# Kernel optimization log

Hardware: AMD Instinct MI355X
Metric: run time of the kernel (lower is better)

The kernel has to match this reference:

```python
import jax, jax.numpy as jnp
import numpy as np

B, N, E = 64, 512, 8192          # graphs, nodes per graph, edges per graph
F_IN, H, C = 128, 128, 10        # in features, hidden, classes
K1, K2 = 256, 128                # dense pool cluster counts: ceil(.5*N), ceil(.5*K1)
EPS = 1e-15


def setup_inputs():
    key = jax.random.key(0)
    keys = jax.random.split(key, 32)
    it = iter(keys)
    def w(shape, fan_in):
        return jax.random.normal(next(it), shape, jnp.float32) / np.sqrt(fan_in)
    x = jax.random.normal(next(it), (B * N, F_IN), jnp.float32)
    src_l = jax.random.randint(next(it), (B, E), 0, N)
    dst_l = jax.random.randint(next(it), (B, E), 0, N)
    off = (jnp.arange(B) * N)[:, None]
    src = (src_l + off).reshape(-1).astype(jnp.int32)
    dst = (dst_l + off).reshape(-1).astype(jnp.int32)
    return dict(
        x=x, src=src, dst=dst,
        conv0_wr=w((F_IN, H), F_IN), conv0_wroot=w((F_IN, H), F_IN), conv0_b=jnp.zeros((H,), jnp.float32),
        sconv2_wr=w((H, H), H), sconv2_wroot=w((H, H), H), sconv2_b=jnp.zeros((H,), jnp.float32),
        sconv3_wr=w((H, H), H), sconv3_wroot=w((H, H), H), sconv3_b=jnp.zeros((H,), jnp.float32),
        sage1_wr=w((H, H), H), sage1_wroot=w((H, H), H), sage1_b=jnp.zeros((H,), jnp.float32),
        sage2_wr=w((H, H), H), sage2_wroot=w((H, H), H), sage2_b=jnp.zeros((H,), jnp.float32),
        pool0_w=w((H, K1), H), pool0_b=jnp.zeros((K1,), jnp.float32),
        pool1_w=w((H, K2), H), pool1_b=jnp.zeros((K2,), jnp.float32),
        p1=w((H,), H), p2=w((H,), H), p3=w((H,), H),
        lin1_1_w=w((2 * H, H), 2 * H), lin1_1_b=jnp.zeros((H,), jnp.float32),
        lin1_w=w((H, H), H), lin1_b=jnp.zeros((H,), jnp.float32),
        lin2_w=w((2 * H, C), 2 * H), lin2_b=jnp.zeros((C,), jnp.float32),
    )


def _graph_conv(x, src, dst, emask, wr, wroot, b, n):
    # PyG GraphConv: lin_rel(sum_j x_j) + lin_root(x_i); invalid edges masked to 0.
    msg = x[src] * emask[:, None]
    agg = jax.ops.segment_sum(msg, dst, num_segments=n)
    return agg @ wr + x @ wroot + b


def _topk_pool(x, score_w, src, dst, emask, n_per_graph, k):
    # TopK pooling (MPoolS): score = x.w/||w||, keep top ratio*n per graph, gate by tanh(score).
    score = x @ score_w / (jnp.linalg.norm(score_w) + 1e-16)
    idx = jax.lax.top_k(score.reshape(B, n_per_graph), k)[1]
    perm = (idx + (jnp.arange(B) * n_per_graph)[:, None]).reshape(-1)
    new_x = x[perm] * jnp.tanh(score[perm])[:, None]
    new_id = jnp.full((B * n_per_graph,), -1, jnp.int32).at[perm].set(
        jnp.arange(B * k, dtype=jnp.int32))
    ns, nd = new_id[src], new_id[dst]
    valid = (ns >= 0) & (nd >= 0) & (emask > 0)
    return new_x, jnp.where(valid, ns, 0), jnp.where(valid, nd, 0), valid.astype(x.dtype)


def _readout(x, k):
    # gmp || gap per graph (nodes are contiguous, k per graph)
    xr = x.reshape(B, k, -1)
    return jnp.concatenate([xr.max(axis=1), xr.mean(axis=1)], axis=-1)


def _dense_sage(x, adj, wr, wroot, b):
    agg = (adj @ x) / jnp.clip(adj.sum(-1, keepdims=True), 1.0, None)
    return agg @ wr + x @ wroot + b


def _dense_mincut_pool(x, adj, s):
    s = jax.nn.softmax(s, axis=-1)
    k = s.shape[-1]
    out = jnp.einsum('bnk,bnf->bkf', s, x)
    out_adj = jnp.einsum('bnk,bnm,bml->bkl', s, adj, s)
    mincut_num = jnp.trace(out_adj, axis1=-2, axis2=-1)
    deg = adj.sum(-1)
    mincut_den = jnp.einsum('bn,bnk,bnk->b', deg, s, s)
    mc = -jnp.mean(mincut_num / (mincut_den + EPS))
    ss = jnp.einsum('bnk,bnl->bkl', s, s)
    ss_n = jnp.linalg.norm(ss, axis=(1, 2), keepdims=True)
    eye = jnp.eye(k, dtype=x.dtype)
    o = jnp.mean(jnp.linalg.norm(ss / (ss_n + EPS) - eye / jnp.sqrt(k), axis=(1, 2)))
    di = jnp.arange(k)
    out_adj = out_adj.at[:, di, di].set(0.0)
    dpool = jnp.sqrt(out_adj.sum(-1)) + EPS
    out_adj = out_adj / dpool[:, :, None] / dpool[:, None, :]
    return out, out_adj, mc, o


def _forward(x, src, dst, conv0_wr, conv0_wroot, conv0_b, sconv2_wr, sconv2_wroot, sconv2_b,
             sconv3_wr, sconv3_wroot, sconv3_b, sage1_wr, sage1_wroot, sage1_b,
             sage2_wr, sage2_wroot, sage2_b, pool0_w, pool0_b, pool1_w, pool1_b,
             p1, p2, p3, lin1_1_w, lin1_1_b, lin1_w, lin1_b, lin2_w, lin2_b):
    relu = jax.nn.relu
    e0 = jnp.ones((src.shape[0],), x.dtype)
    x0 = relu(_graph_conv(x, src, dst, e0, conv0_wr, conv0_wroot, conv0_b, B * N))
    # ---- sparse (MPoolS / top-k) branch, stage 1 ----
    sx, s1, d1, m1 = _topk_pool(x0, p1, src, dst, e0, N, N // 2)
    sx1 = _readout(sx, N // 2)
    # ---- dense (DiffPool-style) branch ----
    xd = x0.reshape(B, N, H)                               # to_dense_batch (full mask)
    g = src // N
    adj = jnp.zeros((B, N, N), x.dtype).at[g, src % N, dst % N].add(1.0)  # to_dense_adj
    s = xd @ pool0_w + pool0_b
    xd, adj, mc, o = _dense_mincut_pool(xd, adj, s)
    xd = relu(_dense_sage(xd, adj, sage1_wr, sage1_wroot, sage1_b))
    s = xd @ pool1_w + pool1_b
    xd, adj, mc2, o2 = _dense_mincut_pool(xd, adj, s)
    mc, o = mc + mc2, o + o2
    xd = _dense_sage(xd, adj, sage2_wr, sage2_wroot, sage2_b)
    xg = relu(xd.mean(axis=1) @ lin1_w + lin1_b)
    # ---- sparse branch, stages 2 and 3 ----
    sx = relu(_graph_conv(sx, s1, d1, m1, sconv2_wr, sconv2_wroot, sconv2_b, B * (N // 2)))
    sx, s2, d2, m2 = _topk_pool(sx, p2, s1, d1, m1, N // 2, N // 4)
    sx2 = _readout(sx, N // 4)
    sx = relu(_graph_conv(sx, s2, d2, m2, sconv3_wr, sconv3_wroot, sconv3_b, B * (N // 4)))
    sx, s3, d3, m3 = _topk_pool(sx, p3, s2, d2, m2, N // 4, N // 8)
    sx3 = _readout(sx, N // 8)
    sxr = relu((sx1 + sx2 + sx3) @ lin1_1_w + lin1_1_b)
    logits = jnp.concatenate([sxr, xg], axis=-1) @ lin2_w + lin2_b
    return logits, mc, o


def reference(x, src, dst, conv0_wr, conv0_wroot, conv0_b, sconv2_wr, sconv2_wroot, sconv2_b,
              sconv3_wr, sconv3_wroot, sconv3_b, sage1_wr, sage1_wroot, sage1_b,
              sage2_wr, sage2_wroot, sage2_b, pool0_w, pool0_b, pool1_w, pool1_b,
              p1, p2, p3, lin1_1_w, lin1_1_b, lin1_w, lin1_b, lin2_w, lin2_b):
    return _forward(x, src, dst, conv0_wr, conv0_wroot, conv0_b, sconv2_wr, sconv2_wroot,
                    sconv2_b, sconv3_wr, sconv3_wroot, sconv3_b, sage1_wr, sage1_wroot,
                    sage1_b, sage2_wr, sage2_wroot, sage2_b, pool0_w, pool0_b, pool1_w,
                    pool1_b, p1, p2, p3, lin1_1_w, lin1_1_b, lin1_w, lin1_b, lin2_w, lin2_b)
```

## Files before the change

kernel.cpp:

```cpp
#include <hip/hip_runtime.h>
#include <math.h>

#define NGRAPH 64
#define NE 524288
#define EPG 8192
#define TSZ 2560

typedef short s16x8 __attribute__((ext_vector_type(8)));
typedef float f32x4 __attribute__((ext_vector_type(4)));

__device__ inline unsigned short f2bf(float f) {
    unsigned int u = __float_as_uint(f);
    return (unsigned short)((u + 0x7FFFu + ((u >> 16) & 1u)) >> 16);
}
__device__ inline float bf2f(unsigned short h) {
    return __uint_as_float((unsigned int)h << 16);
}
__device__ inline unsigned int f2pk(float v) {
    unsigned short h = f2bf(v);
    return (unsigned int)h | ((unsigned int)f2bf(v - bf2f(h)) << 16);
}

__global__ void edge_count2(const int* __restrict__ keyA, int* __restrict__ cntA,
                            const int* __restrict__ keyB, int* __restrict__ cntB) {
    int e = blockIdx.x * 256 + threadIdx.x;
    if (e >= NE) return;
    if (blockIdx.y == 0) atomicAdd(&cntA[keyA[e]], 1);
    else                 atomicAdd(&cntB[keyB[e]], 1);
}

__device__ inline void scan_body(const int* __restrict__ counts, int* __restrict__ offs,
                                 int* __restrict__ cursor, int nPerGraph,
                                 float* __restrict__ degOut, int* s) {
    const int g = blockIdx.x, t = threadIdx.x;
    int v = (t < nPerGraph) ? counts[g * nPerGraph + t] : 0;
    s[t] = v; __syncthreads();
    for (int d = 1; d < 512; d <<= 1) {
        int u = (t >= d) ? s[t - d] : 0;
        __syncthreads();
        s[t] += u;
        __syncthreads();
    }
    if (t < nPerGraph) {
        int o = g * EPG + s[t] - v;
        offs[g * nPerGraph + t] = o;
        cursor[g * nPerGraph + t] = o;
        if (degOut) degOut[g * nPerGraph + t] = (float)v;
    }
}

__global__ __launch_bounds__(512) void scan_offsets(const int* __restrict__ counts,
        int* __restrict__ offs, int* __restrict__ cursor, int nPerGraph,
        float* __restrict__ degOut) {
    __shared__ int s[512];
    scan_body(counts, offs, cursor, nPerGraph, degOut, s);
}

__global__ __launch_bounds__(512) void scan_offsets2(
        const int* __restrict__ cA, int* __restrict__ oA, int* __restrict__ uA,
        const int* __restrict__ cB, int* __restrict__ oB, int* __restrict__ uB,
        int nPerGraph, float* __restrict__ degB) {
    __shared__ int s[512];
    if (blockIdx.y == 0) scan_body(cA, oA, uA, nPerGraph, nullptr, s);
    else                 scan_body(cB, oB, uB, nPerGraph, degB, s);
}

__global__ void edge_fill(const int* __restrict__ key, const int* __restrict__ payload,
                          const float* __restrict__ mask, int* __restrict__ cursor,
                          int* __restrict__ elist) {
    int e = blockIdx.x * 256 + threadIdx.x;
    if (e < NE && (!mask || mask[e] > 0.f)) {
        int p = atomicAdd(&cursor[key[e]], 1);
        elist[p] = payload[e];
    }
}

__global__ void edge_fill2(const int* __restrict__ kA, const int* __restrict__ pA,
                           int* __restrict__ uA, int* __restrict__ eA,
                           const int* __restrict__ kB, const int* __restrict__ pB,
                           int* __restrict__ uB, int* __restrict__ eB) {
    int e = blockIdx.x * 256 + threadIdx.x;
    if (e >= NE) return;
    if (blockIdx.y == 0) { int p = atomicAdd(&uA[kA[e]], 1); eA[p] = pA[e]; }
    else                 { int p = atomicAdd(&uB[kB[e]], 1); eB[p] = pB[e]; }
}

__device__ inline void addpk(float4& acc, uint4 u) {
    acc.x += __uint_as_float(u.x << 16) + __uint_as_float(u.x & 0xffff0000u);
    acc.y += __uint_as_float(u.y << 16) + __uint_as_float(u.y & 0xffff0000u);
    acc.z += __uint_as_float(u.z << 16) + __uint_as_float(u.z & 0xffff0000u);
    acc.w += __uint_as_float(u.w << 16) + __uint_as_float(u.w & 0xffff0000u);
}

__global__ __launch_bounds__(256) void gather_csr(
    const float* __restrict__ xf, const unsigned int* __restrict__ xp, int Fx,
    const int* __restrict__ offs, const int* __restrict__ cnts,
    const int* __restrict__ elist,
    unsigned int* __restrict__ opk,
    int totRows, int rowsPerGraph)
{
    const int gid = (blockIdx.x * 256 + threadIdx.x) >> 5;
    const int lane = threadIdx.x & 31;
    const int csh = (Fx == 256) ? 1 : 0;
    const int rid = gid >> csh;
    const int c0 = (gid & ((1 << csh) - 1)) << 7;
    if (rid >= totRows) return;
    const int row = (rid & 63) * rowsPerGraph + (rid >> 6);
    const int beg = offs[row];
    const int n = cnts[row];
    const long long co = (long long)c0 + (lane << 2);
    float4 acc = make_float4(0.f, 0.f, 0.f, 0.f);
    int j = 0;
    if (xp) {
        for (; j + 4 <= n; j += 4) {
            const int n0 = elist[beg + j], n1 = elist[beg + j + 1];
            const int n2 = elist[beg + j + 2], n3 = elist[beg + j + 3];
            const uint4 u0 = *(const uint4*)&xp[(long long)n0 * Fx + co];
            const uint4 u1 = *(const uint4*)&xp[(long long)n1 * Fx + co];
            const uint4 u2 = *(const uint4*)&xp[(long long)n2 * Fx + co];
            const uint4 u3 = *(const uint4*)&xp[(long long)n3 * Fx + co];
            addpk(acc, u0); addpk(acc, u1); addpk(acc, u2); addpk(acc, u3);
        }
        for (; j < n; ++j)
            addpk(acc, *(const uint4*)&xp[(long long)elist[beg + j] * Fx + co]);
    } else {
        for (; j + 4 <= n; j += 4) {
            const int n0 = elist[beg + j], n1 = elist[beg + j + 1];
            const int n2 = elist[beg + j + 2], n3 = elist[beg + j + 3];
            const float4 v0 = *(const float4*)&xf[(long long)n0 * Fx + co];
            const float4 v1 = *(const float4*)&xf[(long long)n1 * Fx + co];
            const float4 v2 = *(const float4*)&xf[(long long)n2 * Fx + co];
            const float4 v3 = *(const float4*)&xf[(long long)n3 * Fx + co];
            acc.x += v0.x + v1.x + v2.x + v3.x;
            acc.y += v0.y + v1.y + v2.y + v3.y;
            acc.z += v0.z + v1.z + v2.z + v3.z;
            acc.w += v0.w + v1.w + v2.w + v3.w;
        }
        for (; j < n; ++j) {
            const float4 v = *(const float4*)&xf[(long long)elist[beg + j] * Fx + co];
            acc.x += v.x; acc.y += v.y; acc.z += v.z; acc.w += v.w;
        }
    }
    uint4 pk;
    pk.x = f2pk(acc.x); pk.y = f2pk(acc.y); pk.z = f2pk(acc.z); pk.w = f2pk(acc.w);
    *(uint4*)&opk[(long long)row * Fx + co] = pk;
}

struct WSpec {
    const float* w1; const float* w2; int K1; int K2; int Nn;
    unsigned short* oh; unsigned short* ol;
};

__global__ void wconv_all(WSpec s0, WSpec s1, WSpec s2, WSpec s3, WSpec s4, WSpec s5, WSpec s6) {
    WSpec s;
    switch (blockIdx.y) {
        case 0: s = s0; break; case 1: s = s1; break; case 2: s = s2; break;
        case 3: s = s3; break; case 4: s = s4; break; case 5: s = s5; break;
        default: s = s6; break;
    }
    int idx = blockIdx.x * 256 + threadIdx.x;
    int Kt = s.K1 + s.K2;
    if (idx >= s.Nn * Kt) return;
    int n = idx / Kt, k = idx - n * Kt;
    float v = (k < s.K1) ? s.w1[(long long)k * s.Nn + n] : s.w2[(long long)(k - s.K1) * s.Nn + n];
    unsigned short h = f2bf(v);
    s.oh[idx] = h;
    s.ol[idx] = f2bf(v - __uint_as_float((unsigned int)h << 16));
}

__device__ inline void stageN_split(const float* __restrict__ src, int ldk, int k0,
                                    short* lds, int tid) {
    const int r = tid >> 2, kq = (tid & 3) << 3;
    const float* p = src + (long long)r * ldk + k0 + kq;
    float v[8];
    *(float4*)v = *(const float4*)p;
    *(float4*)(v + 4) = *(const float4*)(p + 4);
    s16x8 hv, lv;
    #pragma unroll
    for (int i = 0; i < 8; ++i) {
        unsigned short h = f2bf(v[i]);
        float hf = __uint_as_float((unsigned int)h << 16);
        hv[i] = (short)h;
        lv[i] = (short)f2bf(v[i] - hf);
    }
    *(s16x8*)(lds + r * 40 + kq) = hv;
    *(s16x8*)(lds + TSZ + r * 40 + kq) = lv;
}

__device__ inline void stageN_pk(const unsigned int* __restrict__ src, int ldk, int k0,
                                 short* lds, int tid) {
    const int r = tid >> 2, kq = (tid & 3) << 3;
    const unsigned int* p = src + (long long)r * ldk + k0 + kq;
    uint4 a = *(const uint4*)p;
    uint4 b = *(const uint4*)(p + 4);
    uint4 hw, lw;
    hw.x = (a.x & 0xffffu) | (a.y << 16);
    hw.y = (a.z & 0xffffu) | (a.w << 16);
    hw.z = (b.x & 0xffffu) | (b.y << 16);
    hw.w = (b.z & 0xffffu) | (b.w << 16);
    lw.x = (a.x >> 16) | (a.y & 0xffff0000u);
    lw.y = (a.z >> 16) | (a.w & 0xffff0000u);
    lw.z = (b.x >> 16) | (b.y & 0xffff0000u);
    lw.w = (b.z >> 16) | (b.w & 0xffff0000u);
    *(uint4*)(lds + r * 40 + kq) = hw;
    *(uint4*)(lds + TSZ + r * 40 + kq) = lw;
}

__device__ inline void stageT_pk(const unsigned int* __restrict__ P,
                                 int ldm, int k0, int m0, short* lds, int tid) {
    const int kp = tid >> 4, mc = tid & 15;
    const int k = kp << 1;
    const unsigned int* p0 = P + (long long)(k0 + k) * ldm + m0 + mc;
    const unsigned int* p1 = p0 + ldm;
    #pragma unroll
    for (int i = 0; i < 4; ++i) {
        unsigned int e0 = p0[i << 4], e1 = p1[i << 4];
        const int o = (mc + (i << 4)) * 40 + k;
        *(unsigned int*)(lds + o) = (e0 & 0xffffu) | (e1 << 16);
        *(unsigned int*)(lds + o + TSZ) = (e0 >> 16) | (e1 & 0xffff0000u);
    }
}

__device__ inline void stageT_hi_pk(const unsigned int* __restrict__ P,
                                    int ldm, int k0, int m0, short* lds, int tid) {
    const int kp = tid >> 4, mc = tid & 15;
    const int k = kp << 1;
    const unsigned int* p0 = P + (long long)(k0 + k) * ldm + m0 + mc;
    const unsigned int* p1 = p0 + ldm;
    #pragma unroll
    for (int i = 0; i < 4; ++i) {
        unsigned int e0 = p0[i << 4], e1 = p1[i << 4];
        *(unsigned int*)(lds + (mc + (i << 4)) * 40 + k) = (e0 & 0xffffu) | (e1 << 16);
    }
}

__device__ inline void stageW_split(const unsigned short* __restrict__ wh,
                                    const unsigned short* __restrict__ wl, int ldk,
                                    int n0, int k0, short* lds, int tid) {
    const int r = tid >> 2, kq = (tid & 3) << 3;
    *(s16x8*)(lds + r * 40 + kq) = *(const s16x8*)(wh + (long long)(n0 + r) * ldk + k0 + kq);
    *(s16x8*)(lds + TSZ + r * 40 + kq) = *(const s16x8*)(wl + (long long)(n0 + r) * ldk + k0 + kq);
}

__device__ inline void mfma_split(const short* As, const short* Bs, int wm, int wn,
                                  int l15, int quad, f32x4 (&acc)[2][2]) {
    const int ko = quad << 3;
    s16x8 ah[2], al[2], bh[2], bl[2];
    #pragma unroll
    for (int i = 0; i < 2; ++i) {
        const int ra = (wm + (i << 4) + l15) * 40 + ko;
        const int rb = (wn + (i << 4) + l15) * 40 + ko;
        ah[i] = *(const s16x8*)&As[ra];
        al[i] = *(const s16x8*)&As[TSZ + ra];
        bh[i] = *(const s16x8*)&Bs[rb];
        bl[i] = *(const s16x8*)&Bs[TSZ + rb];
    }
    #pragma unroll
    for (int mi = 0; mi < 2; ++mi)
    #pragma unroll
    for (int ni = 0; ni < 2; ++ni) {
        f32x4 c = acc[mi][ni];
        c = __builtin_amdgcn_mfma_f32_16x16x32_bf16(ah[mi], bh[ni], c, 0, 0, 0);
        c = __builtin_amdgcn_mfma_f32_16x16x32_bf16(ah[mi], bl[ni], c, 0, 0, 0);
        c = __builtin_amdgcn_mfma_f32_16x16x32_bf16(al[mi], bh[ni], c, 0, 0, 0);
        acc[mi][ni] = c;
    }
}

__device__ inline void mfma_hi(const short* As, const short* Bs, int wm, int wn,
                               int l15, int quad, f32x4 (&acc)[2][2]) {
    const int ko = quad << 3;
    s16x8 ah[2], bh[2];
    #pragma unroll
    for (int i = 0; i < 2; ++i) {
        ah[i] = *(const s16x8*)&As[(wm + (i << 4) + l15) * 40 + ko];
        bh[i] = *(const s16x8*)&Bs[(wn + (i << 4) + l15) * 40 + ko];
    }
    #pragma unroll
    for (int mi = 0; mi < 2; ++mi)
    #pragma unroll
    for (int ni = 0; ni < 2; ++ni)
        acc[mi][ni] = __builtin_amdgcn_mfma_f32_16x16x32_bf16(ah[mi], bh[ni], acc[mi][ni], 0, 0, 0);
}

__global__ __launch_bounds__(256) void gemm_aw(
    const unsigned int* __restrict__ A1p, const float* __restrict__ A1f, int K1,
    const unsigned int* __restrict__ A2p, const float* __restrict__ A2f, int K2,
    const unsigned short* __restrict__ Wh, const unsigned short* __restrict__ Wl,
    const float* __restrict__ bias, float* __restrict__ C,
    unsigned int* __restrict__ Cpk,
    int Nn, int doRelu)
{
    __shared__ short As[2 * TSZ], Bs[2 * TSZ];
    const int m0 = blockIdx.y << 6, n0 = blockIdx.x << 6;
    const int tid = threadIdx.x, lane = tid & 63, wv = tid >> 6;
    const int l15 = lane & 15, quad = lane >> 4;
    const int wm = (wv & 1) << 5, wn = (wv >> 1) << 5;
    f32x4 acc[2][2] = {};
    const int Kt = K1 + K2;
    for (int k0 = 0; k0 < Kt; k0 += 32) {
        if (k0 < K1) {
            if (A1p) stageN_pk(A1p + (long long)m0 * K1, K1, k0, As, tid);
            else     stageN_split(A1f + (long long)m0 * K1, K1, k0, As, tid);
        } else {
            if (A2p) stageN_pk(A2p + (long long)m0 * K2, K2, k0 - K1, As, tid);
            else     stageN_split(A2f + (long long)m0 * K2, K2, k0 - K1, As, tid);
        }
        stageW_split(Wh, Wl, Kt, n0, k0, Bs, tid);
        __syncthreads();
        mfma_split(As, Bs, wm, wn, l15, quad, acc);
        __syncthreads();
    }
    #pragma unroll
    for (int mi = 0; mi < 2; ++mi)
    #pragma unroll
    for (int ni = 0; ni < 2; ++ni) {
        const int col = n0 + wn + (ni << 4) + l15;
        const float bv = bias ? bias[col] : 0.f;
        #pragma unroll
        for (int r = 0; r < 4; ++r) {
            const int row = m0 + wm + (mi << 4) + (quad << 2) + r;
            float v = acc[mi][ni][r] + bv;
            if (doRelu) v = fmaxf(v, 0.f);
            if (C)   C[(long long)row * Nn + col] = v;
            if (Cpk) Cpk[(long long)row * Nn + col] = f2pk(v);
        }
    }
}

struct TTSet {
    const unsigned int* Bp;
    float* C; unsigned int* Cpk; float* fro;
    int Nn; int dual;
    long long sB, sC;
};

__global__ __launch_bounds__(256) void gemm_tt(
    const unsigned int* __restrict__ Ap, int Kd, int Mm, long long sA,
    int zsplit, TTSet t0, TTSet t1)
{
    __shared__ short As[2 * TSZ], Bs[2 * TSZ], A2s[TSZ];
    __shared__ float redf[4];
    const int z = blockIdx.x;
    int nz = blockIdx.z;
    const TTSet tt = (nz < zsplit) ? t0 : t1;
    if (blockIdx.z >= zsplit) nz -= zsplit;
    const unsigned int* Apz = Ap + (long long)z * sA;
    const unsigned int* Bpz = tt.Bp + (long long)z * tt.sB;
    const int m0 = blockIdx.y << 6, n0 = nz << 6;
    const int tid = threadIdx.x, lane = tid & 63, wv = tid >> 6;
    const int l15 = lane & 15, quad = lane >> 4;
    const int wm = (wv & 1) << 5, wn = (wv >> 1) << 5;
    const int fw = tt.dual ? ((m0 < n0) ? 2 : ((m0 == n0) ? 1 : 0)) : 0;
    f32x4 acc[2][2] = {};
    f32x4 accA[2][2] = {};
    for (int k0 = 0; k0 < Kd; k0 += 32) {
        stageT_pk(Apz, Mm, k0, m0, As, tid);
        stageT_pk(Bpz, tt.Nn, k0, n0, Bs, tid);
        if (fw) stageT_hi_pk(Apz, Mm, k0, n0, A2s, tid);
        __syncthreads();
        mfma_split(As, Bs, wm, wn, l15, quad, acc);
        if (fw) mfma_hi(As, A2s, wm, wn, l15, quad, accA);
        __syncthreads();
    }
    float* Cp = tt.C ? tt.C + (long long)z * tt.sC : nullptr;
    unsigned int* Ckp = tt.Cpk ? tt.Cpk + (long long)z * tt.sC : nullptr;
    #pragma unroll
    for (int mi = 0; mi < 2; ++mi)
    #pragma unroll
    for (int ni = 0; ni < 2; ++ni) {
        const int col = n0 + wn + (ni << 4) + l15;
        #pragma unroll
        for (int r = 0; r < 4; ++r) {
            const int row = m0 + wm + (mi << 4) + (quad << 2) + r;
            const float v = acc[mi][ni][r];
            if (Cp)  Cp[(long long)row * tt.Nn + col] = v;
            if (Ckp) Ckp[(long long)row * tt.Nn + col] = f2pk(v);
        }
    }
    if (fw) {
        float s = 0.f;
        #pragma unroll
        for (int mi = 0; mi < 2; ++mi)
        #pragma unroll
        for (int ni = 0; ni < 2; ++ni)
        #pragma unroll
        for (int r = 0; r < 4; ++r) s += accA[mi][ni][r] * accA[mi][ni][r];
        s *= (float)fw;
        for (int off = 32; off; off >>= 1) s += __shfl_xor(s, off);
        if (lane == 0) redf[wv] = s;
        __syncthreads();
        if (tid == 0) atomicAdd(&tt.fro[z], redf[0] + redf[1] + redf[2] + redf[3]);
    }
}

__global__ __launch_bounds__(256) void gemm_nt(
    const unsigned short* __restrict__ Ah, const unsigned short* __restrict__ Al,
    const unsigned int* __restrict__ Bp,
    float* __restrict__ C, unsigned int* __restrict__ Cpk,
    const float* __restrict__ rscale, int rsn,
    int Kd, int Nn, long long sA, long long sB, long long sC)
{
    __shared__ short As[2 * TSZ], Bs[2 * TSZ];
    const int z = blockIdx.x;
    const int m0 = blockIdx.y << 6, n0 = blockIdx.z << 6;
    const unsigned short* Aph = Ah + (long long)z * sA;
    const unsigned short* Apl = Al + (long long)z * sA;
    const unsigned int* Bpz = Bp + (long long)z * sB;
    const int tid = threadIdx.x, lane = tid & 63, wv = tid >> 6;
    const int l15 = lane & 15, quad = lane >> 4;
    const int wm = (wv & 1) << 5, wn = (wv >> 1) << 5;
    f32x4 acc[2][2] = {};
    for (int k0 = 0; k0 < Kd; k0 += 32) {
        stageW_split(Aph, Apl, Kd, m0, k0, As, tid);
        stageT_pk(Bpz, Nn, k0, n0, Bs, tid);
        __syncthreads();
        mfma_split(As, Bs, wm, wn, l15, quad, acc);
        __syncthreads();
    }
    #pragma unroll
    for (int mi = 0; mi < 2; ++mi)
    #pragma unroll
    for (int ni = 0; ni < 2; ++ni) {
        const int col = n0 + wn + (ni << 4) + l15;
        #pragma unroll
        for (int r = 0; r < 4; ++r) {
            const int row = m0 + wm + (mi << 4) + (quad << 2) + r;
            float v = acc[mi][ni][r];
            if (rscale) v *= rscale[z * rsn + row];
            if (C)   C[(long long)z * sC + (long long)row * Nn + col] = v;
            if (Cpk) Cpk[(long long)z * sC + (long long)row * Nn + col] = f2pk(v);
        }
    }
}

__global__ __launch_bounds__(256) void softmax_rows_wave(
    const float* __restrict__ sm, int L,
    const float* __restrict__ deg,
    float* __restrict__ rowq2, float* __restrict__ rowdq2, int totRows,
    unsigned int* __restrict__ opk)
{
    const int wid = (blockIdx.x * 256 + threadIdx.x) >> 6;
    const int lane = threadIdx.x & 63;
    if (wid >= totRows) return;
    const float* rowp = sm + (long long)wid * L;
    const int nv = L >> 6;
    float v[4];
    if (nv == 4) {
        float4 t = *(const float4*)&rowp[lane << 2];
        v[0] = t.x; v[1] = t.y; v[2] = t.z; v[3] = t.w;
    } else {
        float2 t = *(const float2*)&rowp[lane << 1];
        v[0] = t.x; v[1] = t.y;
    }
    float mx = v[0];
    for (int i = 1; i < nv; ++i) mx = fmaxf(mx, v[i]);
    for (int off = 32; off; off >>= 1) mx = fmaxf(mx, __shfl_xor(mx, off));
    float s = 0.f;
    for (int i = 0; i < nv; ++i) { v[i] = expf(v[i] - mx); s += v[i]; }
    for (int off = 32; off; off >>= 1) s += __shfl_xor(s, off);
    const float inv = 1.f / s;
    float q2 = 0.f;
    for (int i = 0; i < nv; ++i) { float p = v[i] * inv; v[i] = p; q2 += p * p; }
    const long long rb = (long long)wid * L;
    if (nv == 4) {
        uint4 pk;
        pk.x = f2pk(v[0]); pk.y = f2pk(v[1]); pk.z = f2pk(v[2]); pk.w = f2pk(v[3]);
        *(uint4*)&opk[rb + (lane << 2)] = pk;
    } else {
        uint2 pk;
        pk.x = f2pk(v[0]); pk.y = f2pk(v[1]);
        *(uint2*)&opk[rb + (lane << 1)] = pk;
    }
    for (int off = 32; off; off >>= 1) q2 += __shfl_xor(q2, off);
    if (lane == 0) { rowq2[wid] = q2; rowdq2[wid] = deg[wid] * q2; }
}

__global__ __launch_bounds__(256) void reduce2_pergraph(
    const float* __restrict__ a, const float* __restrict__ b, int rowsPerGraph,
    float* __restrict__ outA, float* __restrict__ outB)
{
    __shared__ float redA[4], redB[4];
    const int g = blockIdx.x, t = threadIdx.x;
    float sa = 0.f, sb = 0.f;
    for (int i = t; i < rowsPerGraph; i += 256) {
        sa += a[g * rowsPerGraph + i];
        if (b) sb += b[g * rowsPerGraph + i];
    }
    for (int off = 32; off; off >>= 1) { sa += __shfl_xor(sa, off); sb += __shfl_xor(sb, off); }
    const int wv = t >> 6;
    if ((t & 63) == 0) { redA[wv] = sa; redB[wv] = sb; }
    __syncthreads();
    if (t == 0) {
        outA[g] = redA[0] + redA[1] + redA[2] + redA[3];
        if (outB) outB[g] = redB[0] + redB[1] + redB[2] + redB[3];
    }
}

__global__ __launch_bounds__(1024) void adjnorm(
    const float* __restrict__ adj, int K,
    float* __restrict__ trace_out,
    float* __restrict__ rowsum, float* __restrict__ rscale,
    unsigned short* __restrict__ oh, unsigned short* __restrict__ ol)
{
    __shared__ float dpoolL[256];
    __shared__ float trL;
    const int g = blockIdx.x, tid = threadIdx.x;
    const int wv = tid >> 6, lane = tid & 63;
    if (tid == 0) trL = 0.f;
    __syncthreads();
    const int rowsPerWave = K >> 4;
    const int nv = K >> 6;
    float trpart = 0.f;
    for (int rr = 0; rr < rowsPerWave; ++rr) {
        const int r = wv * rowsPerWave + rr;
        const float* rowp = adj + (long long)(g * K + r) * K;
        float s = 0.f, dval = 0.f;
        for (int q = 0; q < nv; ++q) {
            int c = lane + (q << 6);
            float v = rowp[c];
            if (c == r) { dval = v; v = 0.f; }
            s += v;
        }
        for (int off = 32; off; off >>= 1) s += __shfl_xor(s, off);
        for (int off = 32; off; off >>= 1) dval += __shfl_xor(dval, off);
        if (lane == 0) { dpoolL[r] = sqrtf(s) + 1e-15f; trpart += dval; }
    }
    if (lane == 0) atomicAdd(&trL, trpart);
    __syncthreads();
    if (tid == 0) trace_out[g] = trL;
    for (int rr = 0; rr < rowsPerWave; ++rr) {
        const int r = wv * rowsPerWave + rr;
        const int wid = g * K + r;
        const float* rowp = adj + (long long)wid * K;
        const float inv_r = 1.f / dpoolL[r];
        float s = 0.f;
        for (int q = 0; q < nv; ++q) {
            int c = lane + (q << 6);
            float a = rowp[c];
            if (c == r) a = 0.f;
            float v = a * inv_r / dpoolL[c];
            s += v;
            unsigned short h = f2bf(v);
            oh[(long long)wid * K + c] = h;
            ol[(long long)wid * K + c] = f2bf(v - bf2f(h));
        }
        for (int off = 32; off; off >>= 1) s += __shfl_xor(s, off);
        if (lane == 0) { rowsum[wid] = s; rscale[wid] = 1.f / fmaxf(s, 1.f); }
    }
}

__global__ __launch_bounds__(512) void topk_fused(
    const float* __restrict__ x, const float* __restrict__ p, int n, int k,
    int* __restrict__ new_id, float* __restrict__ outx,
    float* __restrict__ sxsum, int* __restrict__ cntZero)
{
    __shared__ float sc[512];
    __shared__ int pref[512];
    __shared__ int   selL[256];
    __shared__ float gateL[256];
    __shared__ float red[1024];
    const int g = blockIdx.x, tid = threadIdx.x;
    if (cntZero && tid < k) cntZero[g * k + tid] = 0;
    float myScore = 0.f;
    if (tid < n) {
        const float* xr = x + (long long)(g * n + tid) * 128;
        float pn2 = 0.f, d = 0.f;
        #pragma unroll 4
        for (int f = 0; f < 128; f += 4) {
            float4 pv = *(const float4*)&p[f];
            float4 v = *(const float4*)&xr[f];
            pn2 += pv.x * pv.x + pv.y * pv.y + pv.z * pv.z + pv.w * pv.w;
            d += v.x * pv.x + v.y * pv.y + v.z * pv.z + v.w * pv.w;
        }
        myScore = d / (sqrtf(pn2) + 1e-16f);
        sc[tid] = myScore;
    }
    __syncthreads();
    int keep = 0;
    if (tid < n) {
        const float si = myScore;
        int rank = 0;
        for (int j = 0; j < n; j += 4) {
            float4 s4 = *(const float4*)&sc[j];
            rank += (s4.x > si) || (s4.x == si && (j + 0) < tid);
            rank += (s4.y > si) || (s4.y == si && (j + 1) < tid);
            rank += (s4.z > si) || (s4.z == si && (j + 2) < tid);
            rank += (s4.w > si) || (s4.w == si && (j + 3) < tid);
        }
        keep = rank < k;
    }
    pref[tid] = keep;
    __syncthreads();
    for (int d = 1; d < 512; d <<= 1) {
        int u = (tid >= d) ? pref[tid - d] : 0;
        __syncthreads();
        pref[tid] += u;
        __syncthreads();
    }
    if (tid < n) {
        if (keep) {
            int pos = pref[tid] - 1;
            new_id[g * n + tid] = g * k + pos;
            selL[pos] = g * n + tid;
            gateL[pos] = tanhf(myScore);
        } else new_id[g * n + tid] = -1;
    }
    __syncthreads();
    const int f = tid & 127, grp = tid >> 7;
    float mx = -INFINITY, sm = 0.f;
    for (int r = grp; r < k; r += 4) {
        float v = x[(long long)selL[r] * 128 + f] * gateL[r];
        outx[(long long)(g * k + r) * 128 + f] = v;
        mx = fmaxf(mx, v); sm += v;
    }
    red[grp * 128 + f] = mx;
    red[512 + grp * 128 + f] = sm;
    __syncthreads();
    if (tid < 128) {
        float m = fmaxf(fmaxf(red[f], red[128 + f]), fmaxf(red[256 + f], red[384 + f]));
        float s2 = red[512 + f] + red[640 + f] + red[768 + f] + red[896 + f];
        sxsum[g * 256 + f] += m;
        sxsum[g * 256 + 128 + f] += s2 / k;
    }
}

__global__ void remap_edges_count(const int* __restrict__ s, const int* __restrict__ d,
                                  const float* __restrict__ m, const int* __restrict__ new_id,
                                  int* __restrict__ so, int* __restrict__ do_,
                                  float* __restrict__ mo, int* __restrict__ counts) {
    int e = blockIdx.x * blockDim.x + threadIdx.x;
    if (e >= NE) return;
    int ns = new_id[s[e]], nd = new_id[d[e]];
    bool v = (ns >= 0) && (nd >= 0) && (m ? (m[e] > 0.f) : true);
    so[e] = v ? ns : 0; do_[e] = v ? nd : 0; mo[e] = v ? 1.f : 0.f;
    if (v) atomicAdd(&counts[nd], 1);
}

__global__ void final_head(const float* __restrict__ sxsum, const float* __restrict__ w11,
                           const float* __restrict__ b11,
                           const float* __restrict__ xd2, const float* __restrict__ l1w,
                           const float* __restrict__ l1b,
                           const float* __restrict__ w2, const float* __restrict__ b2,
                           const float* __restrict__ accs, float* __restrict__ out) {
    __shared__ float meanv[128];
    __shared__ float sin_[256];
    __shared__ float cat[256];
    __shared__ float rm[2], ro[2];
    int b = blockIdx.x, t = threadIdx.x;
    {
        float s = 0.f;
        for (int n = 0; n < 128; n++) s += xd2[(long long)(b * 128 + n) * 128 + t];
        meanv[t] = s / 128.f;
    }
    if (b == 0) {
        int wvi = t >> 6, lane = t & 63;
        const float* acc = accs + wvi * 256;
        float sqrtk = wvi ? sqrtf(128.f) : 16.f;
        float numv = acc[lane], denv = acc[64 + lane], trv = acc[128 + lane], frov = acc[192 + lane];
        float mcb = numv / (denv + 1e-15f);
        float ssn = sqrtf(frov) + 1e-15f;
        float ob = sqrtf(fmaxf(frov / (ssn * ssn) - 2.f * trv / (ssn * sqrtk) + 1.f, 0.f));
        for (int off = 32; off; off >>= 1) { mcb += __shfl_down(mcb, off); ob += __shfl_down(ob, off); }
        if (lane == 0) { rm[wvi] = mcb; ro[wvi] = ob; }
        __syncthreads();
        if (t == 0) {
            out[640] = -(rm[0] + rm[1]) / 64.f;
            out[641] = (ro[0] + ro[1]) / 64.f;
        }
    }
    sin_[t] = sxsum[b * 256 + t];
    sin_[t + 128] = sxsum[b * 256 + 128 + t];
    __syncthreads();
    float acc = b11[t];
    for (int i = 0; i < 256; i++) acc += sin_[i] * w11[i * 128 + t];
    cat[t] = fmaxf(acc, 0.f);
    float xga = l1b[t];
    for (int i = 0; i < 128; i++) xga += meanv[i] * l1w[i * 128 + t];
    cat[128 + t] = fmaxf(xga, 0.f);
    __syncthreads();
    if (t < 10) {
        float a = b2[t];
        for (int i = 0; i < 256; i++) a += cat[i] * w2[i * 10 + t];
        out[b * 10 + t] = a;
    }
}

extern "C" void kernel_launch(void* const* d_in, const int* in_sizes, int n_in,
                              void* d_out, int out_size, void* d_ws, size_t ws_size,
                              hipStream_t stream) {
    const float* x         = (const float*)d_in[0];
    const int*   src       = (const int*)d_in[1];
    const int*   dst       = (const int*)d_in[2];
    const float* conv0_wr  = (const float*)d_in[3];
    const float* conv0_wrt = (const float*)d_in[4];
    const float* conv0_b   = (const float*)d_in[5];
    const float* sc2_wr    = (const float*)d_in[6];
    const float* sc2_wrt   = (const float*)d_in[7];
    const float* sc2_b     = (const float*)d_in[8];
    const float* sc3_wr    = (const float*)d_in[9];
    const float* sc3_wrt   = (const float*)d_in[10];
    const float* sc3_b     = (const float*)d_in[11];
    const float* sg1_wr    = (const float*)d_in[12];
    const float* sg1_wrt   = (const float*)d_in[13];
    const float* sg1_b     = (const float*)d_in[14];
    const float* sg2_wr    = (const float*)d_in[15];
    const float* sg2_wrt   = (const float*)d_in[16];
    const float* sg2_b     = (const float*)d_in[17];
    const float* pool0_w   = (const float*)d_in[18];
    const float* pool0_b   = (const float*)d_in[19];
    const float* pool1_w   = (const float*)d_in[20];
    const float* pool1_b   = (const float*)d_in[21];
    const float* p1        = (const float*)d_in[22];
    const float* p2        = (const float*)d_in[23];
    const float* p3        = (const float*)d_in[24];
    const float* l11_w     = (const float*)d_in[25];
    const float* l11_b     = (const float*)d_in[26];
    const float* l1_w      = (const float*)d_in[27];
    const float* l1_b      = (const float*)d_in[28];
    const float* l2_w      = (const float*)d_in[29];
    const float* l2_b      = (const float*)d_in[30];
    float* out = (float*)d_out;

    char* w = (char*)d_ws;
    const unsigned long long MBy = 1ull << 20;
    float* x0    = (float*)(w + 0);
    float* BIG1  = (float*)(w + 16 * MBy);
    float* BIG2  = (float*)(w + 48 * MBy);
    float* agg   = (float*)(w + 80 * MBy);
    float* adj1  = (float*)(w + 104 * MBy);
    int*   s1    = (int*)(w + 120 * MBy);
    int*   d1    = (int*)(w + 122 * MBy);
    float* m1    = (float*)(w + 124 * MBy);
    int*   s2e   = (int*)(w + 126 * MBy);
    int*   d2e   = (int*)(w + 128 * MBy);
    float* m2e   = (float*)(w + 130 * MBy);
    char*  misc  = w + 132 * MBy;
    float* rowq2  = (float*)(misc);
    float* rowdq2 = (float*)(misc + 128 * 1024);
    int*   newid = (int*)(misc + 256 * 1024);
    float* deg   = (float*)(misc + 384 * 1024);
    float* rowsum2 = (float*)(misc + 576 * 1024);
    float* rscale2 = (float*)(misc + 640 * 1024);
    float* rowsum3 = (float*)(misc + 736 * 1024);
    float* rscale3 = (float*)(misc + 768 * 1024);
    float* accs    = (float*)(misc + 800 * 1024);
    float* sxsum   = (float*)(misc + 900 * 1024);

    unsigned short* wt_sg1h   = (unsigned short*)(misc + 1024 * 1024);
    unsigned short* wt_sg1l   = wt_sg1h + 32768;
    unsigned short* wt_sg2h   = wt_sg1l + 32768;
    unsigned short* wt_sg2l   = wt_sg2h + 32768;
    unsigned short* wt_pool0h = wt_sg2l + 32768;
    unsigned short* wt_pool0l = wt_pool0h + 32768;
    unsigned short* wt_pool1h = wt_pool0l + 32768;
    unsigned short* wt_pool1l = wt_pool1h + 32768;
    unsigned short* wt_c0h    = wt_pool1l + 32768;
    unsigned short* wt_c0l    = wt_c0h + 32768;
    unsigned short* wt_sc2h   = wt_c0l + 32768;
    unsigned short* wt_sc2l   = wt_sc2h + 32768;
    unsigned short* wt_sc3h   = wt_sc2l + 32768;
    unsigned short* wt_sc3l   = wt_sc3h + 32768;

    float* s_sm  = BIG1;
    unsigned int* Tbp = (unsigned int*)BIG2;
    float* s2sm  = BIG2 + 4 * 1024 * 1024;
    unsigned int* T2p = (unsigned int*)((char*)BIG2 + 24 * MBy);
    float* adj2b = BIG1 + 1024 * 1024;
    float* xd2   = BIG1 + 2 * 1024 * 1024;
    float* sxA   = BIG1 + 3 * 1024 * 1024;
    float* sxE   = BIG1 + 5 * 1024 * 1024;
    float* sxB   = x0;
    float* sxC   = x0 + 2 * 1024 * 1024;
    float* sxD   = x0 + 3 * 1024 * 1024;

    unsigned int* s_smp = (unsigned int*)(w + 136 * MBy);
    unsigned int* x0p   = (unsigned int*)(w + 168 * MBy);
    unsigned int* ox1p  = (unsigned int*)(w + 184 * MBy);
    unsigned int* xd1p  = (unsigned int*)(w + 192 * MBy);
    unsigned int* s2p   = (unsigned int*)(w + 200 * MBy);
    unsigned int* ox2p  = (unsigned int*)(w + 208 * MBy);
    unsigned short* a1h = (unsigned short*)(w + 212 * MBy);
    unsigned short* a1l = (unsigned short*)(w + 220 * MBy);
    unsigned short* a2h = (unsigned short*)(w + 228 * MBy);
    unsigned short* a2l = (unsigned short*)(w + 230 * MBy);
    unsigned int* AXp   = (unsigned int*)(w + 232 * MBy);
    unsigned int* AXp2  = (unsigned int*)(w + 240 * MBy);

    unsigned int* aggp  = (unsigned int*)agg;
    unsigned int* agg2p = (unsigned int*)agg;
    unsigned int* agg3p = (unsigned int*)agg;

    char* adjc = (char*)adj1;
    int* elA  = (int*)(adjc + 0);
    int* elB  = (int*)(adjc + 2 * MBy);
    int* cntA = (int*)(adjc + 4 * MBy);
    int* cntB = (int*)(adjc + 4 * MBy + 128 * 1024);
    int* offA = (int*)(adjc + 4 * MBy + 256 * 1024);
    int* curA = (int*)(adjc + 4 * MBy + 384 * 1024);
    int* offB = (int*)(adjc + 4 * MBy + 512 * 1024);
    int* curB = (int*)(adjc + 4 * MBy + 640 * 1024);
    char* aggc = (char*)agg;
    int* elC  = (int*)(aggc + 8 * MBy);
    int* elD  = (int*)(aggc + 10 * MBy);
    int* cntC = (int*)(aggc + 12 * MBy);
    int* offC = (int*)(aggc + 12 * MBy + 256 * 1024);
    int* curC = (int*)(aggc + 12 * MBy + 512 * 1024);
    int* cntD = (int*)(aggc + 13 * MBy);
    int* offD = (int*)(aggc + 13 * MBy + 256 * 1024);
    int* curD = (int*)(aggc + 13 * MBy + 512 * 1024);

    hipMemsetAsync(accs, 0, 520 * sizeof(float), stream);
    hipMemsetAsync(sxsum, 0, 16384 * sizeof(float), stream);
    hipMemsetAsync(cntA, 0, 65536 * sizeof(int), stream);

    {
        WSpec a{sg1_wr, sg1_wrt, 128, 128, 128, wt_sg1h, wt_sg1l};
        WSpec b{sg2_wr, sg2_wrt, 128, 128, 128, wt_sg2h, wt_sg2l};
        WSpec c{pool0_w, nullptr, 128, 0, 256, wt_pool0h, wt_pool0l};
        WSpec d{pool1_w, nullptr, 128, 0, 128, wt_pool1h, wt_pool1l};
        WSpec e{conv0_wr, conv0_wrt, 128, 128, 128, wt_c0h, wt_c0l};
        WSpec f{sc2_wr, sc2_wrt, 128, 128, 128, wt_sc2h, wt_sc2l};
        WSpec g{sc3_wr, sc3_wrt, 128, 128, 128, wt_sc3h, wt_sc3l};
        wconv_all<<<dim3(128, 7), 256, 0, stream>>>(a, b, c, d, e, f, g);
    }

    edge_count2<<<dim3(2048, 2), 256, 0, stream>>>(dst, cntA, src, cntB);
    scan_offsets2<<<dim3(64, 2), 512, 0, stream>>>(cntA, offA, curA, cntB, offB, curB, 512, deg);
    edge_fill2<<<dim3(2048, 2), 256, 0, stream>>>(dst, src, curA, elA, src, dst, curB, elB);

    gather_csr<<<4096, 256, 0, stream>>>(x, nullptr, 128, offA, cntA, elA, aggp, 32768, 512);
    gemm_aw<<<dim3(2, 512), 256, 0, stream>>>(aggp, nullptr, 128, nullptr, x, 128,
        wt_c0h, wt_c0l, conv0_b, x0, x0p, 128, 1);

    gemm_aw<<<dim3(4, 512), 256, 0, stream>>>(x0p, nullptr, 128, nullptr, nullptr, 0,
        wt_pool0h, wt_pool0l, pool0_b, s_sm, nullptr, 256, 0);
    softmax_rows_wave<<<8192, 256, 0, stream>>>(s_sm, 256, deg, rowq2, rowdq2, 32768, s_smp);
    reduce2_pergraph<<<64, 256, 0, stream>>>(rowq2, rowdq2, 512, accs + 128, accs + 64);
    gather_csr<<<8192, 256, 0, stream>>>(nullptr, s_smp, 256, offB, cntB, elB, Tbp, 32768, 512);
    {
        TTSet t0{x0p, nullptr, ox1p, nullptr, 128, 0, 512 * 128, 256 * 128};
        TTSet t1{Tbp, adj1, nullptr, accs + 192, 256, 1, 512 * 256, 256 * 256};
        gemm_tt<<<dim3(64, 4, 6), 256, 0, stream>>>(s_smp, 512, 256, 512 * 256, 2, t0, t1);
    }
    adjnorm<<<64, 1024, 0, stream>>>(adj1, 256, accs + 0, rowsum2, rscale2, a1h, a1l);
    gemm_nt<<<dim3(64, 4, 2), 256, 0, stream>>>(a1h, a1l, ox1p, nullptr, AXp, rscale2, 256,
        256, 128, 256 * 256, 256 * 128, 256 * 128);
    gemm_aw<<<dim3(2, 256), 256, 0, stream>>>(AXp, nullptr, 128, ox1p, nullptr, 128,
        wt_sg1h, wt_sg1l, sg1_b, nullptr, xd1p, 128, 1);
    gemm_aw<<<dim3(2, 256), 256, 0, stream>>>(xd1p, nullptr, 128, nullptr, nullptr, 0,
        wt_pool1h, wt_pool1l, pool1_b, s2sm, nullptr, 128, 0);
    softmax_rows_wave<<<4096, 256, 0, stream>>>(s2sm, 128, rowsum2, rowq2, rowdq2, 16384, s2p);
    reduce2_pergraph<<<64, 256, 0, stream>>>(rowq2, rowdq2, 256, accs + 384, accs + 320);
    gemm_nt<<<dim3(64, 4, 2), 256, 0, stream>>>(a1h, a1l, s2p, nullptr, T2p, nullptr, 0,
        256, 128, 256 * 256, 256 * 128, 256 * 128);
    {
        TTSet t0{xd1p, nullptr, ox2p, nullptr, 128, 0, 256 * 128, 128 * 128};
        TTSet t1{T2p, adj2b, nullptr, accs + 448, 128, 1, 256 * 128, 128 * 128};
        gemm_tt<<<dim3(64, 2, 4), 256, 0, stream>>>(s2p, 256, 128, 256 * 128, 2, t0, t1);
    }
    adjnorm<<<64, 1024, 0, stream>>>(adj2b, 128, accs + 256, rowsum3, rscale3, a2h, a2l);
    gemm_nt<<<dim3(64, 2, 2), 256, 0, stream>>>(a2h, a2l, ox2p, nullptr, AXp2, rscale3, 128,
        128, 128, 128 * 128, 128 * 128, 128 * 128);
    gemm_aw<<<dim3(2, 128), 256, 0, stream>>>(AXp2, nullptr, 128, ox2p, nullptr, 128,
        wt_sg2h, wt_sg2l, sg2_b, xd2, nullptr, 128, 0);

    topk_fused<<<64, 512, 0, stream>>>(x0, p1, 512, 256, newid, sxA, sxsum, cntC);
    remap_edges_count<<<2048, 256, 0, stream>>>(src, dst, nullptr, newid, s1, d1, m1, cntC);
    scan_offsets<<<64, 512, 0, stream>>>(cntC, offC, curC, 256, nullptr);
    edge_fill<<<2048, 256, 0, stream>>>(d1, s1, m1, curC, elC);
    gather_csr<<<2048, 256, 0, stream>>>(sxA, nullptr, 128, offC, cntC, elC, agg2p, 16384, 256);
    gemm_aw<<<dim3(2, 256), 256, 0, stream>>>(agg2p, nullptr, 128, nullptr, sxA, 128,
        wt_sc2h, wt_sc2l, sc2_b, sxB, nullptr, 128, 1);
    topk_fused<<<64, 512, 0, stream>>>(sxB, p2, 256, 128, newid, sxC, sxsum, cntD);
    remap_edges_count<<<2048, 256, 0, stream>>>(s1, d1, m1, newid, s2e, d2e, m2e, cntD);
    scan_offsets<<<64, 512, 0, stream>>>(cntD, offD, curD, 128, nullptr);
    edge_fill<<<2048, 256, 0, stream>>>(d2e, s2e, m2e, curD, elD);
    gather_csr<<<1024, 256, 0, stream>>>(sxC, nullptr, 128, offD, cntD, elD, agg3p, 8192, 128);
    gemm_aw<<<dim3(2, 128), 256, 0, stream>>>(agg3p, nullptr, 128, nullptr, sxC, 128,
        wt_sc3h, wt_sc3l, sc3_b, sxD, nullptr, 128, 1);
    topk_fused<<<64, 512, 0, stream>>>(sxD, p3, 128, 64, newid, sxE, sxsum, nullptr);

    final_head<<<64, 128, 0, stream>>>(sxsum, l11_w, l11_b, xd2, l1_w, l1_b,
        l2_w, l2_b, accs, out);
}
```

Before: 645.5 us.

## Prefetch next K-tile into registers during MFMA in the three GEMM kernels

Splits each LDS staging routine into a global-load and an LDS-store half. In gemm_aw, the batched dual GEMM and gemm_nt, the next K-slice is loaded into registers after the first barrier, so the global loads overlap the MFMA work on the current tile. This hides global memory latency without adding LDS. The cost is more live registers per thread, which may reduce occupancy.

New measurement: 695.4 us. 1.08x slower.

```diff
diff --git a/kernel.cpp b/kernel.cpp
--- a/kernel.cpp
+++ b/kernel.cpp
@@ -168,78 +168,75 @@
     s.ol[idx] = f2bf(v - __uint_as_float((unsigned int)h << 16));
 }
 
-__device__ inline void stageN_split(const float* __restrict__ src, int ldk, int k0,
-                                    short* lds, int tid) {
-    const int r = tid >> 2, kq = (tid & 3) << 3;
-    const float* p = src + (long long)r * ldk + k0 + kq;
-    float v[8];
-    *(float4*)v = *(const float4*)p;
-    *(float4*)(v + 4) = *(const float4*)(p + 4);
-    s16x8 hv, lv;
-    #pragma unroll
-    for (int i = 0; i < 8; ++i) {
-        unsigned short h = f2bf(v[i]);
-        float hf = __uint_as_float((unsigned int)h << 16);
-        hv[i] = (short)h;
-        lv[i] = (short)f2bf(v[i] - hf);
-    }
-    *(s16x8*)(lds + r * 40 + kq) = hv;
-    *(s16x8*)(lds + TSZ + r * 40 + kq) = lv;
-}
-
-__device__ inline void stageN_pk(const unsigned int* __restrict__ src, int ldk, int k0,
-                                 short* lds, int tid) {
-    const int r = tid >> 2, kq = (tid & 3) << 3;
-    const unsigned int* p = src + (long long)r * ldk + k0 + kq;
-    uint4 a = *(const uint4*)p;
-    uint4 b = *(const uint4*)(p + 4);
+
+__device__ inline void loadN8(const unsigned int* __restrict__ base, int ldk, int kcol,
+                              int tid, uint4 (&r)[2]) {
+    const int rr = tid >> 2, kq = (tid & 3) << 3;
+    const unsigned int* p = base + (long long)rr * ldk + kcol + kq;
+    r[0] = *(const uint4*)p;
+    r[1] = *(const uint4*)(p + 4);
+}
+__device__ inline void storeN8(short* lds, int tid, uint4 r0, uint4 r1, int pk) {
+    const int rr = tid >> 2, kq = (tid & 3) << 3;
+    if (!pk) {
+        r0.x = f2pk(__uint_as_float(r0.x)); r0.y = f2pk(__uint_as_float(r0.y));
+        r0.z = f2pk(__uint_as_float(r0.z)); r0.w = f2pk(__uint_as_float(r0.w));
+        r1.x = f2pk(__uint_as_float(r1.x)); r1.y = f2pk(__uint_as_float(r1.y));
+        r1.z = f2pk(__uint_as_float(r1.z)); r1.w = f2pk(__uint_as_float(r1.w));
+    }
     uint4 hw, lw;
-    hw.x = (a.x & 0xffffu) | (a.y << 16);
-    hw.y = (a.z & 0xffffu) | (a.w << 16);
-    hw.z = (b.x & 0xffffu) | (b.y << 16);
-    hw.w = (b.z & 0xffffu) | (b.w << 16);
-    lw.x = (a.x >> 16) | (a.y & 0xffff0000u);
-    lw.y = (a.z >> 16) | (a.w & 0xffff0000u);
-    lw.z = (b.x >> 16) | (b.y & 0xffff0000u);
-    lw.w = (b.z >> 16) | (b.w & 0xffff0000u);
-    *(uint4*)(lds + r * 40 + kq) = hw;
-    *(uint4*)(lds + TSZ + r * 40 + kq) = lw;
-}
-
-__device__ inline void stageT_pk(const unsigned int* __restrict__ P,
-                                 int ldm, int k0, int m0, short* lds, int tid) {
+    hw.x = (r0.x & 0xffffu) | (r0.y << 16);
+    hw.y = (r0.z & 0xffffu) | (r0.w << 16);
+    hw.z = (r1.x & 0xffffu) | (r1.y << 16);
+    hw.w = (r1.z & 0xffffu) | (r1.w << 16);
+    lw.x = (r0.x >> 16) | (r0.y & 0xffff0000u);
+    lw.y = (r0.z >> 16) | (r0.w & 0xffff0000u);
+    lw.z = (r1.x >> 16) | (r1.y & 0xffff0000u);
+    lw.w = (r1.z >> 16) | (r1.w & 0xffff0000u);
+    *(uint4*)(lds + rr * 40 + kq) = hw;
+    *(uint4*)(lds + TSZ + rr * 40 + kq) = lw;
+}
+
+__device__ inline void loadW8(const unsigned short* __restrict__ wh,
+                              const unsigned short* __restrict__ wl, int ldk,
+                              int n0, int k0, int tid, uint4 (&r)[2]) {
+    const int rr = tid >> 2, kq = (tid & 3) << 3;
+    r[0] = *(const uint4*)(wh + (long long)(n0 + rr) * ldk + k0 + kq);
+    r[1] = *(const uint4*)(wl + (long long)(n0 + rr) * ldk + k0 + kq);
+}
+__device__ inline void storeW8(short* lds, int tid, const uint4 (&r)[2]) {
+    const int rr = tid >> 2, kq = (tid & 3) << 3;
+    *(uint4*)(lds + rr * 40 + kq) = r[0];
+    *(uint4*)(lds + TSZ + rr * 40 + kq) = r[1];
+}
+
+__device__ inline void loadT8(const unsigned int* __restrict__ P, int ldm, int k0, int m0,
+                              int tid, unsigned int (&r)[8]) {
     const int kp = tid >> 4, mc = tid & 15;
     const int k = kp << 1;
     const unsigned int* p0 = P + (long long)(k0 + k) * ldm + m0 + mc;
     const unsigned int* p1 = p0 + ldm;
     #pragma unroll
+    for (int i = 0; i < 4; ++i) { r[i] = p0[i << 4]; r[4 + i] = p1[i << 4]; }
+}
+__device__ inline void storeT8(short* lds, int tid, const unsigned int (&r)[8]) {
+    const int kp = tid >> 4, mc = tid & 15;
+    const int k = kp << 1;
+    #pragma unroll
     for (int i = 0; i < 4; ++i) {
-        unsigned int e0 = p0[i << 4], e1 = p1[i << 4];
+        unsigned int e0 = r[i], e1 = r[4 + i];
         const int o = (mc + (i << 4)) * 40 + k;
         *(unsigned int*)(lds + o) = (e0 & 0xffffu) | (e1 << 16);
         *(unsigned int*)(lds + o + TSZ) = (e0 >> 16) | (e1 & 0xffff0000u);
     }
 }
-
-__device__ inline void stageT_hi_pk(const unsigned int* __restrict__ P,
-                                    int ldm, int k0, int m0, short* lds, int tid) {
+__device__ inline void storeT8_hi(short* lds, int tid, const unsigned int (&r)[8]) {
     const int kp = tid >> 4, mc = tid & 15;
     const int k = kp << 1;
-    const unsigned int* p0 = P + (long long)(k0 + k) * ldm + m0 + mc;
-    const unsigned int* p1 = p0 + ldm;
-    #pragma unroll
-    for (int i = 0; i < 4; ++i) {
-        unsigned int e0 = p0[i << 4], e1 = p1[i << 4];
-        *(unsigned int*)(lds + (mc + (i << 4)) * 40 + k) = (e0 & 0xffffu) | (e1 << 16);
-    }
-}
-
-__device__ inline void stageW_split(const unsigned short* __restrict__ wh,
-                                    const unsigned short* __restrict__ wl, int ldk,
-                                    int n0, int k0, short* lds, int tid) {
-    const int r = tid >> 2, kq = (tid & 3) << 3;
-    *(s16x8*)(lds + r * 40 + kq) = *(const s16x8*)(wh + (long long)(n0 + r) * ldk + k0 + kq);
-    *(s16x8*)(lds + TSZ + r * 40 + kq) = *(const s16x8*)(wl + (long long)(n0 + r) * ldk + k0 + kq);
+    #pragma unroll
+    for (int i = 0; i < 4; ++i)
+        *(unsigned int*)(lds + (mc + (i << 4)) * 40 + k) =
+            (r[i] & 0xffffu) | (r[4 + i] << 16);
 }
 
 __device__ inline void mfma_split(const short* As, const short* Bs, int wm, int wn,
@@ -298,16 +295,25 @@
     const int wm = (wv & 1) << 5, wn = (wv >> 1) << 5;
     f32x4 acc[2][2] = {};
     const int Kt = K1 + K2;
+    const unsigned int* base1 = A1p ? A1p + (long long)m0 * K1
+                                    : (const unsigned int*)(A1f + (long long)m0 * K1);
+    const unsigned int* base2 = A2p ? A2p + (long long)m0 * K2
+                                    : (const unsigned int*)(A2f + (long long)m0 * K2);
+    const int pk1 = A1p != nullptr, pk2 = A2p != nullptr;
+    uint4 ra[2], rb[2];
+    int curPk = (0 < K1) ? pk1 : pk2;
+    loadN8(base1, K1, 0, tid, ra);
+    loadW8(Wh, Wl, Kt, n0, 0, tid, rb);
     for (int k0 = 0; k0 < Kt; k0 += 32) {
-        if (k0 < K1) {
-            if (A1p) stageN_pk(A1p + (long long)m0 * K1, K1, k0, As, tid);
-            else     stageN_split(A1f + (long long)m0 * K1, K1, k0, As, tid);
-        } else {
-            if (A2p) stageN_pk(A2p + (long long)m0 * K2, K2, k0 - K1, As, tid);
-            else     stageN_split(A2f + (long long)m0 * K2, K2, k0 - K1, As, tid);
-        }
-        stageW_split(Wh, Wl, Kt, n0, k0, Bs, tid);
-        __syncthreads();
+        storeN8(As, tid, ra[0], ra[1], curPk);
+        storeW8(Bs, tid, rb);
+        __syncthreads();
+        const int kn = k0 + 32;
+        if (kn < Kt) {
+            if (kn < K1) { loadN8(base1, K1, kn, tid, ra);      curPk = pk1; }
+            else         { loadN8(base2, K2, kn - K1, tid, ra); curPk = pk2; }
+            loadW8(Wh, Wl, Kt, n0, kn, tid, rb);
+        }
         mfma_split(As, Bs, wm, wn, l15, quad, acc);
         __syncthreads();
     }
@@ -354,11 +360,21 @@
     const int fw = tt.dual ? ((m0 < n0) ? 2 : ((m0 == n0) ? 1 : 0)) : 0;
     f32x4 acc[2][2] = {};
     f32x4 accA[2][2] = {};
+    unsigned int ra[8], rb[8], rh[8];
+    loadT8(Apz, Mm, 0, m0, tid, ra);
+    loadT8(Bpz, tt.Nn, 0, n0, tid, rb);
+    if (fw) loadT8(Apz, Mm, 0, n0, tid, rh);
     for (int k0 = 0; k0 < Kd; k0 += 32) {
-        stageT_pk(Apz, Mm, k0, m0, As, tid);
-        stageT_pk(Bpz, tt.Nn, k0, n0, Bs, tid);
-        if (fw) stageT_hi_pk(Apz, Mm, k0, n0, A2s, tid);
-        __syncthreads();
+        storeT8(As, tid, ra);
+        storeT8(Bs, tid, rb);
+        if (fw) storeT8_hi(A2s, tid, rh);
+        __syncthreads();
+        const int kn = k0 + 32;
+        if (kn < Kd) {
+            loadT8(Apz, Mm, kn, m0, tid, ra);
+            loadT8(Bpz, tt.Nn, kn, n0, tid, rb);
+            if (fw) loadT8(Apz, Mm, kn, n0, tid, rh);
+        }
         mfma_split(As, Bs, wm, wn, l15, quad, acc);
         if (fw) mfma_hi(As, A2s, wm, wn, l15, quad, accA);
         __syncthreads();
@@ -411,10 +427,19 @@
     const int l15 = lane & 15, quad = lane >> 4;
     const int wm = (wv & 1) << 5, wn = (wv >> 1) << 5;
     f32x4 acc[2][2] = {};
+    uint4 ra[2];
+    unsigned int rb[8];
+    loadW8(Aph, Apl, Kd, m0, 0, tid, ra);
+    loadT8(Bpz, Nn, 0, n0, tid, rb);
     for (int k0 = 0; k0 < Kd; k0 += 32) {
-        stageW_split(Aph, Apl, Kd, m0, k0, As, tid);
-        stageT_pk(Bpz, Nn, k0, n0, Bs, tid);
-        __syncthreads();
+        storeW8(As, tid, ra);
+        storeT8(Bs, tid, rb);
+        __syncthreads();
+        const int kn = k0 + 32;
+        if (kn < Kd) {
+            loadW8(Aph, Apl, Kd, m0, kn, tid, ra);
+            loadT8(Bpz, Nn, kn, n0, tid, rb);
+        }
         mfma_split(As, Bs, wm, wn, l15, quad, acc);
         __syncthreads();
     }
```
